# Kernel optimization log

Measured on AMD Instinct MI355X. Metric: run time of the kernel, lower is better.

The kernel has to match this reference:

```python
import jax, jax.numpy as jnp
import numpy as np

N = 50000       # nodes
E = 800000      # edges (avg degree 16)
IN_DIM = 128
H_DIM = 96      # conv='SKP' -> h_dim unchanged
OUT_DIM = 64
NUM_LAYERS = 4
HEADS = 2       # conv='SKP' -> num_heads forced to 2


def setup_inputs() -> dict:
    key = jax.random.key(0)
    ks = jax.random.split(key, 9)
    x = jax.random.normal(ks[0], (N, IN_DIM), jnp.float32)
    edge_index = jax.random.randint(ks[1], (2, E), 0, N, dtype=jnp.int32)
    enc_w = jax.random.normal(ks[2], (IN_DIM, H_DIM), jnp.float32) / np.sqrt(IN_DIM)
    enc_b = jnp.zeros((H_DIM,), jnp.float32)
    dec_w = jax.random.normal(ks[3], (H_DIM, OUT_DIM), jnp.float32) / np.sqrt(H_DIM)
    dec_b = jnp.zeros((OUT_DIM,), jnp.float32)
    # per-layer, per-head linear transforms of the SKP conv
    conv_W = jax.random.normal(ks[4], (NUM_LAYERS, HEADS, H_DIM, H_DIM), jnp.float32) / np.sqrt(H_DIM)
    # per-layer, per-head learnable edge weights (SKP takes num_edges at init)
    conv_ew = jax.random.normal(ks[5], (NUM_LAYERS, HEADS, E), jnp.float32) * 0.1
    return {"x": x, "edge_index": edge_index, "enc_w": enc_w, "enc_b": enc_b,
            "dec_w": dec_w, "dec_b": dec_b, "conv_W": conv_W, "conv_ew": conv_ew}


def _skp_conv(h, src, dst, W, ew):
    # h: [N, d], W: [H, d, d], ew: [H, E]
    # X' = sum_h S_h X W_h  (S_h = learned edge-weighted sparse propagation)
    m = jnp.einsum('nd,hde->hne', h, W)          # [H, N, d] per-head transform
    g = m[:, src, :]                              # [H, E, d] gather at source nodes
    comb = jnp.einsum('he,hed->ed', ew, g)        # weight per edge, sum heads -> [E, d]
    return jax.ops.segment_sum(comb, dst, num_segments=N)  # scatter-add to dest


def reference(x, edge_index, enc_w, enc_b, dec_w, dec_b, conv_W, conv_ew):
    src, dst = edge_index[0], edge_index[1]
    h = jax.nn.relu(x @ enc_w + enc_b)
    for l in range(NUM_LAYERS):
        h = _skp_conv(h, src, dst, conv_W[l], conv_ew[l])
        h = jax.nn.relu(h)   # act=True
    return (h @ dec_w + dec_b, h)
```

## Files before the change

kernel.cpp:

```cpp
#include <hip/hip_runtime.h>

constexpr int IND = 128;
constexpr int HD  = 96;
constexpr int OD  = 64;
constexpr int NL  = 4;

struct F3 { float x, y, z; };

__global__ __launch_bounds__(256) void k_hist(const int* __restrict__ dst, int* __restrict__ deg, int E) {
    int e = blockIdx.x * 256 + threadIdx.x;
    if (e < E) atomicAdd(&deg[dst[e]], 1);
}

__global__ __launch_bounds__(256) void k_scan1(const int* __restrict__ deg, int* __restrict__ bsum, int n) {
    int tid = threadIdx.x;
    int base = blockIdx.x * 1024 + tid * 4;
    int s = 0;
    #pragma unroll
    for (int q = 0; q < 4; ++q) { int i = base + q; if (i < n) s += deg[i]; }
    #pragma unroll
    for (int o = 32; o > 0; o >>= 1) s += __shfl_xor(s, o);
    __shared__ int wsum[4];
    int lane = tid & 63, wid = tid >> 6;
    if (lane == 0) wsum[wid] = s;
    __syncthreads();
    if (tid == 0) bsum[blockIdx.x] = wsum[0] + wsum[1] + wsum[2] + wsum[3];
}

__global__ void k_scan2(const int* __restrict__ bsum, int* __restrict__ boff, int nb,
                        int* __restrict__ row_ptr, int n, int E) {
    int l = threadIdx.x;
    int v = (l < nb) ? bsum[l] : 0;
    int incl = v;
    #pragma unroll
    for (int o = 1; o < 64; o <<= 1) { int t = __shfl_up(incl, o); if (l >= o) incl += t; }
    if (l < nb) boff[l] = incl - v;
    if (l == 0) row_ptr[n] = E;
}

__global__ __launch_bounds__(256) void k_scan3(const int* __restrict__ deg, const int* __restrict__ boff,
                                               int* __restrict__ row_ptr, int n) {
    int tid = threadIdx.x;
    int base = blockIdx.x * 1024 + tid * 4;
    int d[4];
    #pragma unroll
    for (int q = 0; q < 4; ++q) { int i = base + q; d[q] = (i < n) ? deg[i] : 0; }
    int tsum = d[0] + d[1] + d[2] + d[3];
    int incl = tsum;
    #pragma unroll
    for (int o = 1; o < 64; o <<= 1) { int t = __shfl_up(incl, o); if ((tid & 63) >= o) incl += t; }
    __shared__ int wsum[4];
    int lane = tid & 63, wid = tid >> 6;
    if (lane == 63) wsum[wid] = incl;
    __syncthreads();
    int woff = 0;
    for (int w = 0; w < wid; ++w) woff += wsum[w];
    int run = boff[blockIdx.x] + woff + (incl - tsum);
    #pragma unroll
    for (int q = 0; q < 4; ++q) {
        int i = base + q;
        if (i < n) { row_ptr[i] = run; run += d[q]; }
    }
}

__global__ __launch_bounds__(256) void k_fill(const int* __restrict__ src, const int* __restrict__ dst,
                                              const int* __restrict__ row_ptr, int* __restrict__ cursor,
                                              int* __restrict__ srcp, int* __restrict__ eidp, int E) {
    int e = blockIdx.x * 256 + threadIdx.x;
    if (e >= E) return;
    int d = dst[e];
    int pos = atomicAdd(&cursor[d], 1);
    int slot = row_ptr[d] + pos;
    srcp[slot] = src[e];
    eidp[slot] = e;
}

__global__ __launch_bounds__(256) void k_agg(const float* __restrict__ h, const int* __restrict__ row_ptr,
                                             const int* __restrict__ srcp, const int* __restrict__ eidp,
                                             const float* __restrict__ ew0, const float* __restrict__ ew1,
                                             float* __restrict__ A0, float* __restrict__ A1, int n) {
    int g = blockIdx.x * 8 + (threadIdx.x >> 5);
    int lane = threadIdx.x & 31;
    if (g >= n) return;
    int beg = row_ptr[g], end = row_ptr[g + 1];
    float a0x = 0.f, a0y = 0.f, a0z = 0.f;
    float a1x = 0.f, a1y = 0.f, a1z = 0.f;
    int off = lane * 3;
    for (int i = beg; i < end; ++i) {
        int s = srcp[i];
        int e = eidp[i];
        float w0 = ew0[e];
        float w1 = ew1[e];
        F3 v = *(const F3*)(h + (size_t)s * HD + off);
        a0x = fmaf(w0, v.x, a0x); a0y = fmaf(w0, v.y, a0y); a0z = fmaf(w0, v.z, a0z);
        a1x = fmaf(w1, v.x, a1x); a1y = fmaf(w1, v.y, a1y); a1z = fmaf(w1, v.z, a1z);
    }
    float* p0 = A0 + (size_t)g * HD + off;
    p0[0] = a0x; p0[1] = a0y; p0[2] = a0z;
    float* p1 = A1 + (size_t)g * HD + off;
    p1[0] = a1x; p1[1] = a1y; p1[2] = a1z;
}

template<int K, int NO, bool DUAL, bool RELU, bool BIAS>
__global__ __launch_bounds__(512) void k_gemm(const float* __restrict__ A0p, const float* __restrict__ A1p,
                                              const float* __restrict__ W0p, const float* __restrict__ W1p,
                                              const float* __restrict__ bias,
                                              float* __restrict__ out, int nrows) {
    constexpr int BR = 128, KB = 32;
    constexpr int NC = NO / 32;
    __shared__ float sA[KB][BR];
    __shared__ float sW[KB][NO];
    int tid = threadIdx.x;
    int tx = tid & 31;
    int ty = tid >> 5;
    int brow = blockIdx.x * BR;

    float acc[8][NC];
    #pragma unroll
    for (int r = 0; r < 8; ++r)
        #pragma unroll
        for (int j = 0; j < NC; ++j) acc[r][j] = 0.f;

    int srow = tid >> 2;
    int squart = tid & 3;

    #pragma unroll
    for (int head = 0; head < (DUAL ? 2 : 1); ++head) {
        const float* A = (head == 0) ? A0p : A1p;
        const float* W = (head == 0) ? W0p : W1p;
        for (int kc = 0; kc < K; kc += KB) {
            __syncthreads();
            {
                int gr = brow + srow;
                const float* ap = A + (size_t)gr * K + kc;
                #pragma unroll
                for (int i = 0; i < 2; ++i) {
                    int f4 = squart + 4 * i;
                    float4 v = make_float4(0.f, 0.f, 0.f, 0.f);
                    if (gr < nrows) v = *(const float4*)(ap + 4 * f4);
                    int kk = 4 * f4;
                    sA[kk + 0][srow] = v.x;
                    sA[kk + 1][srow] = v.y;
                    sA[kk + 2][srow] = v.z;
                    sA[kk + 3][srow] = v.w;
                }
            }
            {
                const float4* wp4 = (const float4*)(W + kc * NO);
                float4* sw4 = (float4*)&sW[0][0];
                constexpr int TOT4 = KB * NO / 4;
                for (int i = tid; i < TOT4; i += 512) sw4[i] = wp4[i];
            }
            __syncthreads();
            #pragma unroll
            for (int kk = 0; kk < KB; ++kk) {
                float a[8];
                #pragma unroll
                for (int q = 0; q < 2; ++q) {
                    float4 v = *(const float4*)&sA[kk][8 * ty + 4 * q];
                    a[4 * q + 0] = v.x; a[4 * q + 1] = v.y;
                    a[4 * q + 2] = v.z; a[4 * q + 3] = v.w;
                }
                float wv[NC];
                #pragma unroll
                for (int j = 0; j < NC; ++j) wv[j] = sW[kk][tx + 32 * j];
                #pragma unroll
                for (int r = 0; r < 8; ++r)
                    #pragma unroll
                    for (int j = 0; j < NC; ++j)
                        acc[r][j] = fmaf(a[r], wv[j], acc[r][j]);
            }
        }
    }
    #pragma unroll
    for (int r = 0; r < 8; ++r) {
        int gr = brow + 8 * ty + r;
        if (gr < nrows) {
            #pragma unroll
            for (int j = 0; j < NC; ++j) {
                int c = tx + 32 * j;
                float v = acc[r][j];
                if (BIAS) v += bias[c];
                if (RELU) v = fmaxf(v, 0.f);
                out[(size_t)gr * NO + c] = v;
            }
        }
    }
}

extern "C" void kernel_launch(void* const* d_in, const int* in_sizes, int n_in,
                              void* d_out, int out_size, void* d_ws, size_t ws_size,
                              hipStream_t stream) {
    const float* x     = (const float*)d_in[0];
    const int*   ei    = (const int*)  d_in[1];
    const float* enc_w = (const float*)d_in[2];
    const float* enc_b = (const float*)d_in[3];
    const float* dec_w = (const float*)d_in[4];
    const float* dec_b = (const float*)d_in[5];
    const float* convW = (const float*)d_in[6];
    const float* convE = (const float*)d_in[7];

    const int N = in_sizes[0] / IND;
    const int E = in_sizes[1] / 2;
    const int* src = ei;
    const int* dst = ei + E;
    float* fout = (float*)d_out;

    char* wp = (char*)d_ws;
    auto carve = [&](size_t bytes) -> void* {
        void* p = (void*)wp;
        wp += (bytes + 255) & ~(size_t)255;
        return p;
    };
    int* deg     = (int*)carve(2 * (size_t)N * 4);
    int* cursor  = deg + N;
    int* row_ptr = (int*)carve(((size_t)N + 1) * 4);
    int* bsum    = (int*)carve(64 * 4);
    int* boff    = (int*)carve(64 * 4);
    int* srcp    = (int*)carve((size_t)E * 4);
    int* eidp    = (int*)carve((size_t)E * 4);
    float* hbuf  = (float*)carve((size_t)N * HD * 4);
    float* Ag0   = (float*)carve((size_t)N * HD * 4);
    float* Ag1   = (float*)carve((size_t)N * HD * 4);

    hipMemsetAsync(deg, 0, 2 * (size_t)N * 4, stream);

    int ebl = (E + 255) / 256;
    int nb  = (N + 1023) / 1024;
    k_hist<<<ebl, 256, 0, stream>>>(dst, deg, E);
    k_scan1<<<nb, 256, 0, stream>>>(deg, bsum, N);
    k_scan2<<<1, 64, 0, stream>>>(bsum, boff, nb, row_ptr, N, E);
    k_scan3<<<nb, 256, 0, stream>>>(deg, boff, row_ptr, N);
    k_fill<<<ebl, 256, 0, stream>>>(src, dst, row_ptr, cursor, srcp, eidp, E);

    int gbl = (N + 127) / 128;
    k_gemm<IND, HD, false, true, true><<<gbl, 512, 0, stream>>>(x, nullptr, enc_w, nullptr, enc_b, hbuf, N);

    float* hfin = fout + (size_t)N * OD;
    for (int l = 0; l < NL; ++l) {
        const float* W0 = convW + ((size_t)l * 2 + 0) * HD * HD;
        const float* W1 = convW + ((size_t)l * 2 + 1) * HD * HD;
        const float* e0 = convE + ((size_t)l * 2 + 0) * E;
        const float* e1 = convE + ((size_t)l * 2 + 1) * E;
        k_agg<<<(N + 7) / 8, 256, 0, stream>>>(hbuf, row_ptr, srcp, eidp, e0, e1, Ag0, Ag1, N);
        float* ho = (l == NL - 1) ? hfin : hbuf;
        k_gemm<HD, HD, true, true, false><<<gbl, 512, 0, stream>>>(Ag0, Ag1, W0, W1, nullptr, ho, N);
    }
    k_gemm<HD, OD, false, false, true><<<gbl, 512, 0, stream>>>(hfin, nullptr, dec_w, nullptr, dec_b, fout, N);
}
```

Measured before the change: 732.5 us.

## Fuse aggregation with per-head GEMM and pre-permute edge weights into CSR order

Merges the per-layer edge aggregation and the dual-head transform into one kernel. Each block aggregates 64 destination rows into shared memory and then multiplies them by both head weight matrices, which removes the round trip through the two N×96 intermediate buffers. Edge weights for all layers are gathered once during CSR fill into float2 arrays in slot order, so the indirect eid lookup and its two scattered loads go away. The encoder and decoder now use a simpler GEMM that reads weights straight from global memory instead of staging them in shared memory. In exchange, the GEMM stage has less reuse per block, and aggregation and GEMM no longer overlap across separate kernels.

```diff
diff --git a/kernel.cpp b/kernel.cpp
--- a/kernel.cpp
+++ b/kernel.cpp
@@ -65,124 +65,159 @@
 
 __global__ __launch_bounds__(256) void k_fill(const int* __restrict__ src, const int* __restrict__ dst,
                                               const int* __restrict__ row_ptr, int* __restrict__ cursor,
-                                              int* __restrict__ srcp, int* __restrict__ eidp, int E) {
+                                              const float* __restrict__ convE,
+                                              int* __restrict__ srcp, float2* __restrict__ ewp, int E) {
     int e = blockIdx.x * 256 + threadIdx.x;
     if (e >= E) return;
     int d = dst[e];
     int pos = atomicAdd(&cursor[d], 1);
     int slot = row_ptr[d] + pos;
     srcp[slot] = src[e];
-    eidp[slot] = e;
-}
-
-__global__ __launch_bounds__(256) void k_agg(const float* __restrict__ h, const int* __restrict__ row_ptr,
-                                             const int* __restrict__ srcp, const int* __restrict__ eidp,
-                                             const float* __restrict__ ew0, const float* __restrict__ ew1,
-                                             float* __restrict__ A0, float* __restrict__ A1, int n) {
-    int g = blockIdx.x * 8 + (threadIdx.x >> 5);
-    int lane = threadIdx.x & 31;
-    if (g >= n) return;
-    int beg = row_ptr[g], end = row_ptr[g + 1];
-    float a0x = 0.f, a0y = 0.f, a0z = 0.f;
-    float a1x = 0.f, a1y = 0.f, a1z = 0.f;
-    int off = lane * 3;
-    for (int i = beg; i < end; ++i) {
-        int s = srcp[i];
-        int e = eidp[i];
-        float w0 = ew0[e];
-        float w1 = ew1[e];
-        F3 v = *(const F3*)(h + (size_t)s * HD + off);
-        a0x = fmaf(w0, v.x, a0x); a0y = fmaf(w0, v.y, a0y); a0z = fmaf(w0, v.z, a0z);
-        a1x = fmaf(w1, v.x, a1x); a1y = fmaf(w1, v.y, a1y); a1z = fmaf(w1, v.z, a1z);
-    }
-    float* p0 = A0 + (size_t)g * HD + off;
-    p0[0] = a0x; p0[1] = a0y; p0[2] = a0z;
-    float* p1 = A1 + (size_t)g * HD + off;
-    p1[0] = a1x; p1[1] = a1y; p1[2] = a1z;
-}
-
-template<int K, int NO, bool DUAL, bool RELU, bool BIAS>
-__global__ __launch_bounds__(512) void k_gemm(const float* __restrict__ A0p, const float* __restrict__ A1p,
-                                              const float* __restrict__ W0p, const float* __restrict__ W1p,
-                                              const float* __restrict__ bias,
-                                              float* __restrict__ out, int nrows) {
-    constexpr int BR = 128, KB = 32;
-    constexpr int NC = NO / 32;
-    __shared__ float sA[KB][BR];
-    __shared__ float sW[KB][NO];
-    int tid = threadIdx.x;
+    #pragma unroll
+    for (int l = 0; l < NL; ++l) {
+        float2 w;
+        w.x = convE[(size_t)(2 * l)     * E + e];
+        w.y = convE[(size_t)(2 * l + 1) * E + e];
+        ewp[(size_t)l * E + slot] = w;
+    }
+}
+
+constexpr int BR = 64;
+constexpr int PIT = HD + 4;
+
+__global__ __launch_bounds__(256) void k_layer(const float* __restrict__ hin,
+                                               const int* __restrict__ row_ptr,
+                                               const int* __restrict__ srcp,
+                                               const float2* __restrict__ ewp,
+                                               const float* __restrict__ W,
+                                               float* __restrict__ hout, int n) {
+    __shared__ float sA0[BR][PIT];
+    __shared__ float sA1[BR][PIT];
+    int tid = threadIdx.x;
+    int brow = blockIdx.x * BR;
+
+    {
+        int grp = tid >> 5;
+        int lane = tid & 31;
+        int off = lane * 3;
+        for (int q = 0; q < 8; ++q) {
+            int r = grp * 8 + q;
+            int g = brow + r;
+            float a0x = 0.f, a0y = 0.f, a0z = 0.f;
+            float a1x = 0.f, a1y = 0.f, a1z = 0.f;
+            if (g < n) {
+                int i = row_ptr[g], end = row_ptr[g + 1];
+                for (; i + 2 <= end; i += 2) {
+                    int s0 = srcp[i];
+                    int s1 = srcp[i + 1];
+                    float2 w0 = ewp[i];
+                    float2 w1 = ewp[i + 1];
+                    F3 v0 = *(const F3*)(hin + (size_t)s0 * HD + off);
+                    F3 v1 = *(const F3*)(hin + (size_t)s1 * HD + off);
+                    a0x = fmaf(w0.x, v0.x, a0x); a0y = fmaf(w0.x, v0.y, a0y); a0z = fmaf(w0.x, v0.z, a0z);
+                    a1x = fmaf(w0.y, v0.x, a1x); a1y = fmaf(w0.y, v0.y, a1y); a1z = fmaf(w0.y, v0.z, a1z);
+                    a0x = fmaf(w1.x, v1.x, a0x); a0y = fmaf(w1.x, v1.y, a0y); a0z = fmaf(w1.x, v1.z, a0z);
+                    a1x = fmaf(w1.y, v1.x, a1x); a1y = fmaf(w1.y, v1.y, a1y); a1z = fmaf(w1.y, v1.z, a1z);
+                }
+                if (i < end) {
+                    int s0 = srcp[i];
+                    float2 w0 = ewp[i];
+                    F3 v0 = *(const F3*)(hin + (size_t)s0 * HD + off);
+                    a0x = fmaf(w0.x, v0.x, a0x); a0y = fmaf(w0.x, v0.y, a0y); a0z = fmaf(w0.x, v0.z, a0z);
+                    a1x = fmaf(w0.y, v0.x, a1x); a1y = fmaf(w0.y, v0.y, a1y); a1z = fmaf(w0.y, v0.z, a1z);
+                }
+            }
+            sA0[r][off] = a0x; sA0[r][off + 1] = a0y; sA0[r][off + 2] = a0z;
+            sA1[r][off] = a1x; sA1[r][off + 1] = a1y; sA1[r][off + 2] = a1z;
+        }
+    }
+    __syncthreads();
+
     int tx = tid & 31;
     int ty = tid >> 5;
-    int brow = blockIdx.x * BR;
-
-    float acc[8][NC];
-    #pragma unroll
-    for (int r = 0; r < 8; ++r)
-        #pragma unroll
-        for (int j = 0; j < NC; ++j) acc[r][j] = 0.f;
-
-    int srow = tid >> 2;
-    int squart = tid & 3;
-
-    #pragma unroll
-    for (int head = 0; head < (DUAL ? 2 : 1); ++head) {
-        const float* A = (head == 0) ? A0p : A1p;
-        const float* W = (head == 0) ? W0p : W1p;
-        for (int kc = 0; kc < K; kc += KB) {
-            __syncthreads();
-            {
-                int gr = brow + srow;
-                const float* ap = A + (size_t)gr * K + kc;
-                #pragma unroll
-                for (int i = 0; i < 2; ++i) {
-                    int f4 = squart + 4 * i;
-                    float4 v = make_float4(0.f, 0.f, 0.f, 0.f);
-                    if (gr < nrows) v = *(const float4*)(ap + 4 * f4);
-                    int kk = 4 * f4;
-                    sA[kk + 0][srow] = v.x;
-                    sA[kk + 1][srow] = v.y;
-                    sA[kk + 2][srow] = v.z;
-                    sA[kk + 3][srow] = v.w;
-                }
-            }
-            {
-                const float4* wp4 = (const float4*)(W + kc * NO);
-                float4* sw4 = (float4*)&sW[0][0];
-                constexpr int TOT4 = KB * NO / 4;
-                for (int i = tid; i < TOT4; i += 512) sw4[i] = wp4[i];
-            }
-            __syncthreads();
-            #pragma unroll
-            for (int kk = 0; kk < KB; ++kk) {
-                float a[8];
-                #pragma unroll
-                for (int q = 0; q < 2; ++q) {
-                    float4 v = *(const float4*)&sA[kk][8 * ty + 4 * q];
-                    a[4 * q + 0] = v.x; a[4 * q + 1] = v.y;
-                    a[4 * q + 2] = v.z; a[4 * q + 3] = v.w;
-                }
-                float wv[NC];
-                #pragma unroll
-                for (int j = 0; j < NC; ++j) wv[j] = sW[kk][tx + 32 * j];
-                #pragma unroll
-                for (int r = 0; r < 8; ++r)
-                    #pragma unroll
-                    for (int j = 0; j < NC; ++j)
-                        acc[r][j] = fmaf(a[r], wv[j], acc[r][j]);
+    float acc[8][3];
+    #pragma unroll
+    for (int r = 0; r < 8; ++r) { acc[r][0] = 0.f; acc[r][1] = 0.f; acc[r][2] = 0.f; }
+
+    #pragma unroll
+    for (int head = 0; head < 2; ++head) {
+        const float* Wh = W + (size_t)head * HD * HD;
+        const float (*sAh)[PIT] = head ? sA1 : sA0;
+        #pragma unroll 4
+        for (int kk = 0; kk < HD; ++kk) {
+            F3 wv = *(const F3*)(Wh + (size_t)kk * HD + 3 * tx);
+            float a[8];
+            #pragma unroll
+            for (int r = 0; r < 8; ++r) a[r] = sAh[8 * ty + r][kk];
+            #pragma unroll
+            for (int r = 0; r < 8; ++r) {
+                acc[r][0] = fmaf(a[r], wv.x, acc[r][0]);
+                acc[r][1] = fmaf(a[r], wv.y, acc[r][1]);
+                acc[r][2] = fmaf(a[r], wv.z, acc[r][2]);
             }
         }
     }
     #pragma unroll
     for (int r = 0; r < 8; ++r) {
         int gr = brow + 8 * ty + r;
-        if (gr < nrows) {
+        if (gr < n) {
+            float* op = hout + (size_t)gr * HD + 3 * tx;
+            op[0] = fmaxf(acc[r][0], 0.f);
+            op[1] = fmaxf(acc[r][1], 0.f);
+            op[2] = fmaxf(acc[r][2], 0.f);
+        }
+    }
+}
+
+template<int K, int NO, bool RELU>
+__global__ __launch_bounds__(256) void k_mlp(const float* __restrict__ A,
+                                             const float* __restrict__ W,
+                                             const float* __restrict__ bias,
+                                             float* __restrict__ out, int n) {
+    constexpr int P = K + 4;
+    constexpr int NC = NO / 32;
+    __shared__ float sA[64][P];
+    int tid = threadIdx.x;
+    int brow = blockIdx.x * 64;
+    constexpr int F4 = K / 4;
+    for (int i = tid; i < 64 * F4; i += 256) {
+        int r = i / F4, c4 = i % F4;
+        int gr = brow + r;
+        float4 v = make_float4(0.f, 0.f, 0.f, 0.f);
+        if (gr < n) v = *(const float4*)(A + (size_t)gr * K + 4 * c4);
+        *(float4*)&sA[r][4 * c4] = v;
+    }
+    __syncthreads();
+    int tx = tid & 31;
+    int ty = tid >> 5;
+    float acc[8][NC];
+    #pragma unroll
+    for (int r = 0; r < 8; ++r)
+        #pragma unroll
+        for (int j = 0; j < NC; ++j) acc[r][j] = 0.f;
+    #pragma unroll 4
+    for (int kk = 0; kk < K; ++kk) {
+        float wv[NC];
+        #pragma unroll
+        for (int j = 0; j < NC; ++j) wv[j] = W[(size_t)kk * NO + NC * tx + j];
+        float a[8];
+        #pragma unroll
+        for (int r = 0; r < 8; ++r) a[r] = sA[8 * ty + r][kk];
+        #pragma unroll
+        for (int r = 0; r < 8; ++r)
+            #pragma unroll
+            for (int j = 0; j < NC; ++j) acc[r][j] = fmaf(a[r], wv[j], acc[r][j]);
+    }
+    #pragma unroll
+    for (int r = 0; r < 8; ++r) {
+        int gr = brow + 8 * ty + r;
+        if (gr < n) {
+            float* op = out + (size_t)gr * NO + NC * tx;
             #pragma unroll
             for (int j = 0; j < NC; ++j) {
-                int c = tx + 32 * j;
-                float v = acc[r][j];
-                if (BIAS) v += bias[c];
+                float v = acc[r][j] + bias[NC * tx + j];
                 if (RELU) v = fmaxf(v, 0.f);
-                out[(size_t)gr * NO + c] = v;
+                op[j] = v;
             }
         }
     }
@@ -212,16 +247,14 @@
         wp += (bytes + 255) & ~(size_t)255;
         return p;
     };
-    int* deg     = (int*)carve(2 * (size_t)N * 4);
-    int* cursor  = deg + N;
-    int* row_ptr = (int*)carve(((size_t)N + 1) * 4);
-    int* bsum    = (int*)carve(64 * 4);
-    int* boff    = (int*)carve(64 * 4);
-    int* srcp    = (int*)carve((size_t)E * 4);
-    int* eidp    = (int*)carve((size_t)E * 4);
-    float* hbuf  = (float*)carve((size_t)N * HD * 4);
-    float* Ag0   = (float*)carve((size_t)N * HD * 4);
-    float* Ag1   = (float*)carve((size_t)N * HD * 4);
+    int*    deg     = (int*)carve(2 * (size_t)N * 4);
+    int*    cursor  = deg + N;
+    int*    row_ptr = (int*)carve(((size_t)N + 1) * 4);
+    int*    bsum    = (int*)carve(64 * 4);
+    int*    boff    = (int*)carve(64 * 4);
+    int*    srcp    = (int*)carve((size_t)E * 4);
+    float2* ewp     = (float2*)carve((size_t)NL * E * 8);
+    float*  hbuf    = (float*)carve((size_t)N * HD * 4);
 
     hipMemsetAsync(deg, 0, 2 * (size_t)N * 4, stream);
 
@@ -231,20 +264,19 @@
     k_scan1<<<nb, 256, 0, stream>>>(deg, bsum, N);
     k_scan2<<<1, 64, 0, stream>>>(bsum, boff, nb, row_ptr, N, E);
     k_scan3<<<nb, 256, 0, stream>>>(deg, boff, row_ptr, N);
-    k_fill<<<ebl, 256, 0, stream>>>(src, dst, row_ptr, cursor, srcp, eidp, E);
-
-    int gbl = (N + 127) / 128;
-    k_gemm<IND, HD, false, true, true><<<gbl, 512, 0, stream>>>(x, nullptr, enc_w, nullptr, enc_b, hbuf, N);
-
+    k_fill<<<ebl, 256, 0, stream>>>(src, dst, row_ptr, cursor, convE, srcp, ewp, E);
+
+    int gbl = (N + 63) / 64;
     float* hfin = fout + (size_t)N * OD;
+
+    k_mlp<IND, HD, true><<<gbl, 256, 0, stream>>>(x, enc_w, enc_b, hfin, N);
+
+    float* bufs[2] = { hfin, hbuf };
     for (int l = 0; l < NL; ++l) {
-        const float* W0 = convW + ((size_t)l * 2 + 0) * HD * HD;
-        const float* W1 = convW + ((size_t)l * 2 + 1) * HD * HD;
-        const float* e0 = convE + ((size_t)l * 2 + 0) * E;
-        const float* e1 = convE + ((size_t)l * 2 + 1) * E;
-        k_agg<<<(N + 7) / 8, 256, 0, stream>>>(hbuf, row_ptr, srcp, eidp, e0, e1, Ag0, Ag1, N);
-        float* ho = (l == NL - 1) ? hfin : hbuf;
-        k_gemm<HD, HD, true, true, false><<<gbl, 512, 0, stream>>>(Ag0, Ag1, W0, W1, nullptr, ho, N);
-    }
-    k_gemm<HD, OD, false, false, true><<<gbl, 512, 0, stream>>>(hfin, nullptr, dec_w, nullptr, dec_b, fout, N);
-}
+        const float* Wl = convW + (size_t)l * 2 * HD * HD;
+        const float* hi = bufs[l & 1];
+        float*       ho = bufs[(l + 1) & 1];
+        k_layer<<<gbl, 256, 0, stream>>>(hi, row_ptr, srcp, ewp + (size_t)l * E, Wl, ho, N);
+    }
+    k_mlp<HD, OD, false><<<gbl, 256, 0, stream>>>(hfin, dec_w, dec_b, fout, N);
+}
```

New measurement: 835.1 us. 14.0% more time.
